# Kernel optimization log

Measured on AMD Instinct MI355X. Metric: run time of the kernel, lower is better.

Reference implementation:

```python
import jax, jax.numpy as jnp
import numpy as np

D = 256; NH = 8; NLEV = 4; NPTS = 4; DH = D // NH
DFFN = 1024; B = 8; LQ = 900
SHAPES = np.array([[100, 100], [50, 50], [25, 25], [13, 13]], dtype=np.int64)
STARTS = np.concatenate([[0], np.cumsum(SHAPES[:, 0] * SHAPES[:, 1])[:-1]]).astype(np.int64)
LEN = int((SHAPES[:, 0] * SHAPES[:, 1]).sum())


def _ln(x, w, b, eps=1e-5):
    m = x.mean(-1, keepdims=True)
    v = ((x - m) ** 2).mean(-1, keepdims=True)
    return (x - m) / jnp.sqrt(v + eps) * w + b


def _msdeform(q, ref, src, val_w, val_b, off_w, off_b, aw_w, aw_b, op_w, op_b):
    # Multi-scale deformable attention (Deformable DETR core), grid_sample
    # bilinear / zeros padding / align_corners=False semantics.
    Bq, Lq = q.shape[0], q.shape[1]
    value = (src @ val_w + val_b).reshape(Bq, -1, NH, DH)
    off = (q @ off_w + off_b).reshape(Bq, Lq, NH, NLEV, NPTS, 2)
    aw = jax.nn.softmax((q @ aw_w + aw_b).reshape(Bq, Lq, NH, NLEV * NPTS), -1)
    aw = aw.reshape(Bq, Lq, NH, NLEV, NPTS)
    norm = jnp.asarray(SHAPES[:, ::-1].copy(), dtype=q.dtype)  # (W_l, H_l)
    loc = ref[:, :, None, :, None, :] + off / norm[None, None, None, :, None, :]
    out = jnp.zeros((Bq, Lq, NH, DH), q.dtype)
    for l in range(NLEV):
        Hl, Wl = int(SHAPES[l, 0]), int(SHAPES[l, 1]); s = int(STARTS[l])
        v = value[:, s:s + Hl * Wl]                  # [B, Hl*Wl, NH, DH]
        lx = loc[:, :, :, l, :, 0] * Wl - 0.5        # align_corners=False pixel coords
        ly = loc[:, :, :, l, :, 1] * Hl - 0.5        # [B, Lq, NH, NPTS]
        x0 = jnp.floor(lx); y0 = jnp.floor(ly)
        fx = lx - x0; fy = ly - y0
        x0 = x0.astype(jnp.int32); y0 = y0.astype(jnp.int32)
        samp = jnp.zeros((Bq, Lq, NH, NPTS, DH), q.dtype)
        for dx, dy in ((0, 0), (1, 0), (0, 1), (1, 1)):
            xi = x0 + dx; yi = y0 + dy
            w = (fx if dx else 1.0 - fx) * (fy if dy else 1.0 - fy)
            valid = (xi >= 0) & (xi < Wl) & (yi >= 0) & (yi < Hl)
            idx = jnp.clip(yi, 0, Hl - 1) * Wl + jnp.clip(xi, 0, Wl - 1)
            idx_f = idx.transpose(0, 1, 3, 2).reshape(Bq, Lq * NPTS, NH)
            g = jnp.take_along_axis(v, idx_f[..., None], axis=1)
            g = g.reshape(Bq, Lq, NPTS, NH, DH).transpose(0, 1, 3, 2, 4)
            samp = samp + jnp.where(valid, w, 0.0)[..., None] * g
        out = out + jnp.sum(samp * aw[:, :, :, l, :, None], axis=3)
    return out.reshape(Bq, Lq, D) @ op_w + op_b


def _forward(tgt, query_pos, reference_points, src, qkv_w, qkv_b, out_w, out_b,
             ln2_w, ln2_b, val_w, val_b, off_w, off_b, aw_w, aw_b, op_w, op_b,
             ln1_w, ln1_b, w1, b1, w2, b2, ln3_w, ln3_b):
    Bq, Lq, _ = tgt.shape
    # --- self attention: q=k=tgt+pos, value=tgt (eval mode, no dropout) ---
    q = tgt + query_pos
    wq, wk, wv = qkv_w[:, :D], qkv_w[:, D:2 * D], qkv_w[:, 2 * D:]
    bq, bk, bv = qkv_b[:D], qkv_b[D:2 * D], qkv_b[2 * D:]
    qh = (q @ wq + bq).reshape(Bq, Lq, NH, DH)
    kh = (q @ wk + bk).reshape(Bq, Lq, NH, DH)
    vh = (tgt @ wv + bv).reshape(Bq, Lq, NH, DH)
    scores = jnp.einsum('bqhd,bkhd->bhqk', qh, kh) / jnp.sqrt(jnp.asarray(DH, tgt.dtype))
    attn = jax.nn.softmax(scores, -1)
    sa = jnp.einsum('bhqk,bkhd->bqhd', attn, vh).reshape(Bq, Lq, D) @ out_w + out_b
    tgt = _ln(tgt + sa, ln2_w, ln2_b)
    # --- multi-scale deformable cross attention ---
    ca = _msdeform(tgt + query_pos, reference_points, src,
                   val_w, val_b, off_w, off_b, aw_w, aw_b, op_w, op_b)
    tgt = _ln(tgt + ca, ln1_w, ln1_b)
    # --- FFN ---
    ff = jax.nn.relu(tgt @ w1 + b1) @ w2 + b2
    return _ln(tgt + ff, ln3_w, ln3_b)


def setup_inputs():
    key = jax.random.key(0)
    ks = jax.random.split(key, 16)
    s = 0.02
    return {
        'tgt': jax.random.normal(ks[0], (B, LQ, D), jnp.float32),
        'query_pos': jax.random.normal(ks[1], (B, LQ, D), jnp.float32),
        'reference_points': jax.random.uniform(ks[2], (B, LQ, NLEV, 2), jnp.float32),
        'src': jax.random.normal(ks[3], (B, LEN, D), jnp.float32),
        'spatial_shapes': jnp.asarray(SHAPES),
        'level_start_index': jnp.asarray(STARTS),
        'qkv_w': jax.random.normal(ks[4], (D, 3 * D), jnp.float32) * s,
        'qkv_b': jnp.zeros((3 * D,), jnp.float32),
        'out_w': jax.random.normal(ks[5], (D, D), jnp.float32) * s,
        'out_b': jnp.zeros((D,), jnp.float32),
        'ln2_w': jnp.ones((D,), jnp.float32), 'ln2_b': jnp.zeros((D,), jnp.float32),
        'val_w': jax.random.normal(ks[6], (D, D), jnp.float32) * s,
        'val_b': jnp.zeros((D,), jnp.float32),
        'off_w': jax.random.normal(ks[7], (D, NH * NLEV * NPTS * 2), jnp.float32) * s,
        'off_b': jax.random.normal(ks[8], (NH * NLEV * NPTS * 2,), jnp.float32) * 0.5,
        'aw_w': jax.random.normal(ks[9], (D, NH * NLEV * NPTS), jnp.float32) * s,
        'aw_b': jnp.zeros((NH * NLEV * NPTS,), jnp.float32),
        'op_w': jax.random.normal(ks[10], (D, D), jnp.float32) * s,
        'op_b': jnp.zeros((D,), jnp.float32),
        'ln1_w': jnp.ones((D,), jnp.float32), 'ln1_b': jnp.zeros((D,), jnp.float32),
        'w1': jax.random.normal(ks[11], (D, DFFN), jnp.float32) * s,
        'b1': jnp.zeros((DFFN,), jnp.float32),
        'w2': jax.random.normal(ks[12], (DFFN, D), jnp.float32) * s,
        'b2': jnp.zeros((D,), jnp.float32),
        'ln3_w': jnp.ones((D,), jnp.float32), 'ln3_b': jnp.zeros((D,), jnp.float32),
    }


def reference(tgt, query_pos, reference_points, src, spatial_shapes, level_start_index,
              qkv_w, qkv_b, out_w, out_b, ln2_w, ln2_b, val_w, val_b, off_w, off_b,
              aw_w, aw_b, op_w, op_b, ln1_w, ln1_b, w1, b1, w2, b2, ln3_w, ln3_b):
    return _forward(tgt, query_pos, reference_points, src, qkv_w, qkv_b, out_w, out_b,
                    ln2_w, ln2_b, val_w, val_b, off_w, off_b, aw_w, aw_b, op_w, op_b,
                    ln1_w, ln1_b, w1, b1, w2, b2, ln3_w, ln3_b)
```

## Files before the change

kernel.cpp:

```cpp
#include <hip/hip_runtime.h>
#include <math.h>

#define Dm    256
#define NHm   8
#define DHm   32
#define NLEVm 4
#define NPTSm 4
#define DFFNm 1024
#define Bm    8
#define LQm   900
#define LENm  13294
#define MQ    (Bm * LQm)
#define MV    (Bm * LENm)
#define MQP   7296
#define MVP   106368
#define LQP   960

typedef __attribute__((ext_vector_type(8))) short short8;
typedef __attribute__((ext_vector_type(4))) float f32x4;

__device__ __forceinline__ unsigned short f2bf(float f) {
    unsigned int b = __float_as_uint(f);
    unsigned int r = (b + 0x7FFFu + ((b >> 16) & 1u)) >> 16;
    return (unsigned short)r;
}
__device__ __forceinline__ float bf2f(unsigned short u) {
    return __uint_as_float(((unsigned int)u) << 16);
}

__global__ __launch_bounds__(256) void prep0(const float* __restrict__ tgt,
                                             const float* __restrict__ qpos,
                                             unsigned short* __restrict__ tgtb,
                                             unsigned short* __restrict__ qb,
                                             int n4, int n4pad) {
    int i = blockIdx.x * blockDim.x + threadIdx.x;
    int stride = gridDim.x * blockDim.x;
    for (; i < n4pad; i += stride) {
        ushort4 ut, uq;
        if (i < n4) {
            float4 x = reinterpret_cast<const float4*>(tgt)[i];
            float4 y = reinterpret_cast<const float4*>(qpos)[i];
            ut.x = f2bf(x.x); ut.y = f2bf(x.y); ut.z = f2bf(x.z); ut.w = f2bf(x.w);
            uq.x = f2bf(x.x + y.x); uq.y = f2bf(x.y + y.y);
            uq.z = f2bf(x.z + y.z); uq.w = f2bf(x.w + y.w);
        } else {
            ut.x = ut.y = ut.z = ut.w = 0;
            uq.x = uq.y = uq.z = uq.w = 0;
        }
        reinterpret_cast<ushort4*>(tgtb)[i] = ut;
        reinterpret_cast<ushort4*>(qb)[i] = uq;
    }
}

__device__ __forceinline__ void wt_tile(const float* __restrict__ W,
                                        unsigned short* __restrict__ BT,
                                        int N, int K, int n0, int k0, int t,
                                        float (*tile)[65]) {
    #pragma unroll
    for (int r0 = 0; r0 < 64; r0 += 16) {
        int r = r0 + (t >> 4);
        int c = (t & 15) * 4;
        float4 v = *reinterpret_cast<const float4*>(W + (size_t)(k0 + r) * N + n0 + c);
        tile[r][c + 0] = v.x; tile[r][c + 1] = v.y; tile[r][c + 2] = v.z; tile[r][c + 3] = v.w;
    }
    __syncthreads();
    #pragma unroll
    for (int s = t; s < 512; s += 256) {
        int r = s >> 3, c8 = (s & 7) * 8;
        short8 u;
        #pragma unroll
        for (int j = 0; j < 8; ++j) u[j] = (short)f2bf(tile[c8 + j][r]);
        *reinterpret_cast<short8*>(BT + (size_t)(n0 + r) * K + k0 + c8) = u;
    }
}

__global__ __launch_bounds__(256) void wt_all(
        const float* __restrict__ qkv_w, const float* __restrict__ out_w,
        const float* __restrict__ val_w, const float* __restrict__ off_w,
        const float* __restrict__ aw_w,  const float* __restrict__ op_w,
        const float* __restrict__ w1,    const float* __restrict__ w2,
        unsigned short* __restrict__ BT_qkv, unsigned short* __restrict__ BT_out,
        unsigned short* __restrict__ BT_val, unsigned short* __restrict__ BT_off,
        unsigned short* __restrict__ BT_aw,  unsigned short* __restrict__ BT_op,
        unsigned short* __restrict__ BT_w1,  unsigned short* __restrict__ BT_w2) {
    __shared__ float tile[64][65];
    int bid = blockIdx.x;
    int t = threadIdx.x;
    const float* W; unsigned short* BT; int N, K, idx;
    if      (bid < 48)  { W = qkv_w; BT = BT_qkv; N = 768;  K = 256;  idx = bid; }
    else if (bid < 64)  { W = out_w; BT = BT_out; N = 256;  K = 256;  idx = bid - 48; }
    else if (bid < 80)  { W = val_w; BT = BT_val; N = 256;  K = 256;  idx = bid - 64; }
    else if (bid < 96)  { W = off_w; BT = BT_off; N = 256;  K = 256;  idx = bid - 80; }
    else if (bid < 104) { W = aw_w;  BT = BT_aw;  N = 128;  K = 256;  idx = bid - 96; }
    else if (bid < 120) { W = op_w;  BT = BT_op;  N = 256;  K = 256;  idx = bid - 104; }
    else if (bid < 184) { W = w1;    BT = BT_w1;  N = 1024; K = 256;  idx = bid - 120; }
    else                { W = w2;    BT = BT_w2;  N = 256;  K = 1024; idx = bid - 184; }
    int nt = N / 64;
    int n0 = (idx % nt) * 64, k0 = (idx / nt) * 64;
    wt_tile(W, BT, N, K, n0, k0, t, tile);
}

__device__ __forceinline__ void mfma_step(const unsigned short* Ac, const unsigned short* Bc,
                                          int wr, int wc, int l, f32x4 acc[4][4]) {
    short8 af[4], bfr[4];
    #pragma unroll
    for (int m = 0; m < 4; ++m)
        af[m] = *(const short8*)(Ac + (wr + m * 16 + (l & 15)) * 32 + (l >> 4) * 8);
    #pragma unroll
    for (int n = 0; n < 4; ++n)
        bfr[n] = *(const short8*)(Bc + (wc + n * 16 + (l & 15)) * 32 + (l >> 4) * 8);
    #pragma unroll
    for (int m = 0; m < 4; ++m)
        #pragma unroll
        for (int n = 0; n < 4; ++n)
            acc[m][n] = __builtin_amdgcn_mfma_f32_16x16x32_bf16(af[m], bfr[n], acc[m][n], 0, 0, 0);
}

template <int RELU, int OBF>
__global__ __launch_bounds__(256) void bgemm(int M, int N, int K,
        const unsigned short* __restrict__ A,
        const unsigned short* __restrict__ BT,
        const float* __restrict__ bias, const float* __restrict__ bias2,
        float* __restrict__ Cf, float* __restrict__ Cf2,
        unsigned short* __restrict__ Cb, int ldc) {
    __shared__ __align__(16) unsigned short As[2][128 * 32];
    __shared__ __align__(16) unsigned short Bs[2][128 * 32];
    int t = threadIdx.x;
    int l = t & 63;
    int w = t >> 6;
    int row0 = blockIdx.x * 128, col0 = blockIdx.y * 128;
    int wr = (w >> 1) * 64, wc = (w & 1) * 64;
    f32x4 acc[4][4];
    #pragma unroll
    for (int m = 0; m < 4; ++m)
        #pragma unroll
        for (int n = 0; n < 4; ++n) acc[m][n] = (f32x4){0.f, 0.f, 0.f, 0.f};

    int s0 = t, s1 = t + 256;
    const unsigned short* Ag = A + (size_t)row0 * K;
    const unsigned short* Bg = BT + (size_t)col0 * K;
    const unsigned short* a0p = Ag + (size_t)(s0 >> 2) * K + (s0 & 3) * 8;
    const unsigned short* a1p = Ag + (size_t)(s1 >> 2) * K + (s1 & 3) * 8;
    const unsigned short* b0p = Bg + (size_t)(s0 >> 2) * K + (s0 & 3) * 8;
    const unsigned short* b1p = Bg + (size_t)(s1 >> 2) * K + (s1 & 3) * 8;

    short8 ra0 = *(const short8*)(a0p);
    short8 ra1 = *(const short8*)(a1p);
    short8 rb0 = *(const short8*)(b0p);
    short8 rb1 = *(const short8*)(b1p);

    int cur = 0;
    for (int k0 = 0; k0 < K; k0 += 32) {
        unsigned short* Ac = As[cur];
        unsigned short* Bc = Bs[cur];
        *(short8*)(Ac + s0 * 8) = ra0;
        *(short8*)(Ac + s1 * 8) = ra1;
        *(short8*)(Bc + s0 * 8) = rb0;
        *(short8*)(Bc + s1 * 8) = rb1;
        if (k0 + 32 < K) {
            ra0 = *(const short8*)(a0p + k0 + 32);
            ra1 = *(const short8*)(a1p + k0 + 32);
            rb0 = *(const short8*)(b0p + k0 + 32);
            rb1 = *(const short8*)(b1p + k0 + 32);
        }
        __syncthreads();
        mfma_step(Ac, Bc, wr, wc, l, acc);
        cur ^= 1;
    }

    int cr = (l >> 4) * 4;
    int cc = l & 15;
    #pragma unroll
    for (int m = 0; m < 4; ++m) {
        #pragma unroll
        for (int n = 0; n < 4; ++n) {
            int col = col0 + wc + n * 16 + cc;
            if (OBF == 3) {
                float bv = (col < 256) ? bias[col] : bias2[col - 256];
                #pragma unroll
                for (int j = 0; j < 4; ++j) {
                    int r = row0 + wr + m * 16 + cr + j;
                    if (r < M) {
                        float v = acc[m][n][j] + bv;
                        if (col < 256) Cf[(size_t)r * 256 + col] = v;
                        else           Cf2[(size_t)r * 128 + (col - 256)] = v;
                    }
                }
            } else {
                float bv = bias[col];
                #pragma unroll
                for (int j = 0; j < 4; ++j) {
                    int r = row0 + wr + m * 16 + cr + j;
                    if (r < M) {
                        float v = acc[m][n][j] + bv;
                        if (RELU) v = fmaxf(v, 0.f);
                        if (OBF) Cb[(size_t)r * ldc + col] = f2bf(v);
                        else     Cf[(size_t)r * ldc + col] = v;
                    }
                }
            }
        }
    }
}

__global__ __launch_bounds__(256) void fused_gemms(
        const float* __restrict__ src, const unsigned short* __restrict__ BT_val,
        const float* __restrict__ val_b, unsigned short* __restrict__ value_bf,
        const unsigned short* __restrict__ Qbf, const unsigned short* __restrict__ BT_qkv,
        const float* __restrict__ qkv_b, unsigned short* __restrict__ qk_bf,
        const unsigned short* __restrict__ tgt_bf, unsigned short* __restrict__ Vt) {
    __shared__ __align__(16) unsigned short As[2][128 * 32];
    __shared__ __align__(16) unsigned short Bs[2][128 * 32];
    int bid = blockIdx.x;
    int t = threadIdx.x;

    if (bid >= 2004) {
        int i = (bid - 2004) * 256 + t;
        int row = i / 60, c = 900 + (i % 60);
        Vt[(size_t)row * LQP + c] = 0;
        return;
    }

    int l = t & 63, w = t >> 6;
    int wr = (w >> 1) * 64, wc = (w & 1) * 64;
    int s0 = t, s1 = t + 256;
    f32x4 acc[4][4];
    #pragma unroll
    for (int m = 0; m < 4; ++m)
        #pragma unroll
        for (int n = 0; n < 4; ++n) acc[m][n] = (f32x4){0.f, 0.f, 0.f, 0.f};
    int cr = (l >> 4) * 4;
    int cc = l & 15;

    if (bid < 1662) {
        int row0 = (bid % 831) * 128, col0 = (bid / 831) * 128;
        int r0c = min(row0 + (s0 >> 2), MV - 1);
        int r1c = min(row0 + (s1 >> 2), MV - 1);
        const float* a0p = src + (size_t)r0c * 256 + (s0 & 3) * 8;
        const float* a1p = src + (size_t)r1c * 256 + (s1 & 3) * 8;
        const unsigned short* Bg = BT_val + (size_t)col0 * 256;
        const unsigned short* b0p = Bg + (size_t)(s0 >> 2) * 256 + (s0 & 3) * 8;
        const unsigned short* b1p = Bg + (size_t)(s1 >> 2) * 256 + (s1 & 3) * 8;

        float4 fa0 = *(const float4*)(a0p);
        float4 fa1 = *(const float4*)(a0p + 4);
        float4 fb0 = *(const float4*)(a1p);
        float4 fb1 = *(const float4*)(a1p + 4);
        short8 rb0 = *(const short8*)(b0p);
        short8 rb1 = *(const short8*)(b1p);

        int cur = 0;
        for (int k0 = 0; k0 < 256; k0 += 32) {
            unsigned short* Ac = As[cur];
            unsigned short* Bc = Bs[cur];
            short8 ra0, ra1;
            ra0[0] = (short)f2bf(fa0.x); ra0[1] = (short)f2bf(fa0.y);
            ra0[2] = (short)f2bf(fa0.z); ra0[3] = (short)f2bf(fa0.w);
            ra0[4] = (short)f2bf(fa1.x); ra0[5] = (short)f2bf(fa1.y);
            ra0[6] = (short)f2bf(fa1.z); ra0[7] = (short)f2bf(fa1.w);
            ra1[0] = (short)f2bf(fb0.x); ra1[1] = (short)f2bf(fb0.y);
            ra1[2] = (short)f2bf(fb0.z); ra1[3] = (short)f2bf(fb0.w);
            ra1[4] = (short)f2bf(fb1.x); ra1[5] = (short)f2bf(fb1.y);
            ra1[6] = (short)f2bf(fb1.z); ra1[7] = (short)f2bf(fb1.w);
            *(short8*)(Ac + s0 * 8) = ra0;
            *(short8*)(Ac + s1 * 8) = ra1;
            *(short8*)(Bc + s0 * 8) = rb0;
            *(short8*)(Bc + s1 * 8) = rb1;
            if (k0 + 32 < 256) {
                fa0 = *(const float4*)(a0p + k0 + 32);
                fa1 = *(const float4*)(a0p + k0 + 36);
                fb0 = *(const float4*)(a1p + k0 + 32);
                fb1 = *(const float4*)(a1p + k0 + 36);
                rb0 = *(const short8*)(b0p + k0 + 32);
                rb1 = *(const short8*)(b1p + k0 + 32);
            }
            __syncthreads();
            mfma_step(Ac, Bc, wr, wc, l, acc);
            cur ^= 1;
        }
        #pragma unroll
        for (int m = 0; m < 4; ++m) {
            #pragma unroll
            for (int n = 0; n < 4; ++n) {
                int col = col0 + wc + n * 16 + cc;
                float bv = val_b[col];
                #pragma unroll
                for (int j = 0; j < 4; ++j) {
                    int r = row0 + wr + m * 16 + cr + j;
                    if (r < MV)
                        value_bf[(size_t)r * 256 + col] = f2bf(acc[m][n][j] + bv);
                }
            }
        }
    } else {
        bool is_qk = (bid < 1890);
        int idx = is_qk ? (bid - 1662) : (bid - 1890);
        int row0 = (idx % 57) * 128;
        int col0 = (idx / 57) * 128;
        const unsigned short* A  = is_qk ? Qbf : tgt_bf;
        const unsigned short* BT = is_qk ? BT_qkv : (BT_qkv + 512 * 256);
        const float* bias        = is_qk ? qkv_b : (qkv_b + 512);

        const unsigned short* Ag = A + (size_t)row0 * 256;
        const unsigned short* Bg = BT + (size_t)col0 * 256;
        const unsigned short* a0p = Ag + (size_t)(s0 >> 2) * 256 + (s0 & 3) * 8;
        const unsigned short* a1p = Ag + (size_t)(s1 >> 2) * 256 + (s1 & 3) * 8;
        const unsigned short* b0p = Bg + (size_t)(s0 >> 2) * 256 + (s0 & 3) * 8;
        const unsigned short* b1p = Bg + (size_t)(s1 >> 2) * 256 + (s1 & 3) * 8;

        short8 ra0 = *(const short8*)(a0p);
        short8 ra1 = *(const short8*)(a1p);
        short8 rb0 = *(const short8*)(b0p);
        short8 rb1 = *(const short8*)(b1p);

        int cur = 0;
        for (int k0 = 0; k0 < 256; k0 += 32) {
            unsigned short* Ac = As[cur];
            unsigned short* Bc = Bs[cur];
            *(short8*)(Ac + s0 * 8) = ra0;
            *(short8*)(Ac + s1 * 8) = ra1;
            *(short8*)(Bc + s0 * 8) = rb0;
            *(short8*)(Bc + s1 * 8) = rb1;
            if (k0 + 32 < 256) {
                ra0 = *(const short8*)(a0p + k0 + 32);
                ra1 = *(const short8*)(a1p + k0 + 32);
                rb0 = *(const short8*)(b0p + k0 + 32);
                rb1 = *(const short8*)(b1p + k0 + 32);
            }
            __syncthreads();
            mfma_step(Ac, Bc, wr, wc, l, acc);
            cur ^= 1;
        }

        if (is_qk) {
            #pragma unroll
            for (int m = 0; m < 4; ++m) {
                #pragma unroll
                for (int n = 0; n < 4; ++n) {
                    int col = col0 + wc + n * 16 + cc;
                    float bv = bias[col];
                    #pragma unroll
                    for (int j = 0; j < 4; ++j) {
                        int r = row0 + wr + m * 16 + cr + j;
                        if (r < MQ)
                            qk_bf[(size_t)r * 512 + col] = f2bf(acc[m][n][j] + bv);
                    }
                }
            }
        } else {
            #pragma unroll
            for (int m = 0; m < 4; ++m) {
                #pragma unroll
                for (int n = 0; n < 4; ++n) {
                    int col = col0 + wc + n * 16 + cc;
                    float bv = bias[col];
                    int r0 = row0 + wr + m * 16 + cr;
                    if (r0 < MQ) {
                        int bb = r0 / 900;
                        int q = r0 - bb * 900;
                        ushort4 u;
                        u.x = f2bf(acc[m][n][0] + bv);
                        u.y = f2bf(acc[m][n][1] + bv);
                        u.z = f2bf(acc[m][n][2] + bv);
                        u.w = f2bf(acc[m][n][3] + bv);
                        *reinterpret_cast<ushort4*>(Vt + ((size_t)(bb * 256 + col)) * LQP + q) = u;
                    }
                }
            }
        }
    }
}

__global__ __launch_bounds__(256) void flash_mfma(const unsigned short* __restrict__ qk,
                                                  const unsigned short* __restrict__ vt,
                                                  unsigned short* __restrict__ out) {
    __shared__ unsigned short P_lds[4][16][72];
    int t = threadIdx.x;
    int l = t & 63, w = t >> 6;
    int lr = l & 15, lg = l >> 4;
    int qt = blockIdx.x, h = blockIdx.y, b = blockIdx.z;
    const float scale = 0.17677669529663687f;

    short8 qf = *(const short8*)(qk + (size_t)(b * LQm + qt * 64 + w * 16 + lr) * 512 + h * 32 + lg * 8);

    f32x4 accO[2];
    accO[0] = (f32x4){0.f, 0.f, 0.f, 0.f};
    accO[1] = (f32x4){0.f, 0.f, 0.f, 0.f};
    float mrow[4] = {-1e30f, -1e30f, -1e30f, -1e30f};
    float lrow[4] = {0.f, 0.f, 0.f, 0.f};
    const f32x4 zero = (f32x4){0.f, 0.f, 0.f, 0.f};
    const unsigned short* vtb = vt + ((size_t)(b * 256 + h * 32)) * LQP;

    for (int kt = 0; kt < 15; ++kt) {
        int k0 = kt * 64;
        f32x4 sfr[4];
        #pragma unroll
        for (int ks = 0; ks < 4; ++ks) {
            short8 kf = *(const short8*)(qk + (size_t)(b * LQm + k0 + ks * 16 + lr) * 512 + 256 + h * 32 + lg * 8);
            sfr[ks] = __builtin_amdgcn_mfma_f32_16x16x32_bf16(qf, kf, zero, 0, 0, 0);
        }
        float sv[4][4];
        #pragma unroll
        for (int ks = 0; ks < 4; ++ks) {
            bool valid = (k0 + ks * 16 + lr) < LQm;
            #pragma unroll
            for (int j = 0; j < 4; ++j)
                sv[ks][j] = valid ? sfr[ks][j] * scale : -1e30f;
        }
        float tm[4], newm[4], rr[4], ps[4];
        #pragma unroll
        for (int j = 0; j < 4; ++j)
            tm[j] = fmaxf(fmaxf(sv[0][j], sv[1][j]), fmaxf(sv[2][j], sv[3][j]));
        #pragma unroll
        for (int msk = 1; msk <= 8; msk <<= 1) {
            #pragma unroll
            for (int j = 0; j < 4; ++j) tm[j] = fmaxf(tm[j], __shfl_xor(tm[j], msk));
        }
        #pragma unroll
        for (int j = 0; j < 4; ++j) {
            newm[j] = fmaxf(mrow[j], tm[j]);
            rr[j] = __expf(mrow[j] - newm[j]);
            mrow[j] = newm[j];
            ps[j] = 0.f;
        }
        float pv[4][4];
        #pragma unroll
        for (int ks = 0; ks < 4; ++ks)
            #pragma unroll
            for (int j = 0; j < 4; ++j) {
                pv[ks][j] = __expf(sv[ks][j] - newm[j]);
                ps[j] += pv[ks][j];
            }
        #pragma unroll
        for (int msk = 1; msk <= 8; msk <<= 1) {
            #pragma unroll
            for (int j = 0; j < 4; ++j) ps[j] += __shfl_xor(ps[j], msk);
        }
        #pragma unroll
        for (int j = 0; j < 4; ++j) lrow[j] = lrow[j] * rr[j] + ps[j];
        #pragma unroll
        for (int n = 0; n < 2; ++n)
            #pragma unroll
            for (int j = 0; j < 4; ++j) accO[n][j] *= rr[j];
        #pragma unroll
        for (int ks = 0; ks < 4; ++ks)
            #pragma unroll
            for (int j = 0; j < 4; ++j)
                P_lds[w][lg * 4 + j][ks * 16 + lr] = f2bf(pv[ks][j]);
        #pragma unroll
        for (int kh2 = 0; kh2 < 2; ++kh2) {
            short8 pf = *(const short8*)(&P_lds[w][lr][kh2 * 32 + lg * 8]);
            #pragma unroll
            for (int n = 0; n < 2; ++n) {
                short8 vf = *(const short8*)(vtb + (size_t)(n * 16 + lr) * LQP + k0 + kh2 * 32 + lg * 8);
                accO[n] = __builtin_amdgcn_mfma_f32_16x16x32_bf16(pf, vf, accO[n], 0, 0, 0);
            }
        }
    }
    float inv[4];
    #pragma unroll
    for (int j = 0; j < 4; ++j) inv[j] = 1.0f / lrow[j];
    #pragma unroll
    for (int n = 0; n < 2; ++n)
        #pragma unroll
        for (int j = 0; j < 4; ++j) {
            int q = qt * 64 + w * 16 + lg * 4 + j;
            if (q < LQm)
                out[(size_t)(b * LQm + q) * 256 + h * 32 + n * 16 + lr] = f2bf(accO[n][j] * inv[j]);
        }
}

template <int DUAL, int QP>
__global__ __launch_bounds__(256) void add_ln_kernel(const float* __restrict__ x,
                                                     const float* __restrict__ r,
                                                     const float* __restrict__ w,
                                                     const float* __restrict__ b,
                                                     const float* __restrict__ qpos,
                                                     float* __restrict__ out,
                                                     unsigned short* __restrict__ outb,
                                                     unsigned short* __restrict__ outq) {
    int row = blockIdx.x * 4 + (threadIdx.x >> 6);
    int lane = threadIdx.x & 63;
    size_t i4 = (size_t)row * 64 + lane;
    float4 xv = reinterpret_cast<const float4*>(x)[i4];
    float4 rv = reinterpret_cast<const float4*>(r)[i4];
    float4 v = make_float4(xv.x + rv.x, xv.y + rv.y, xv.z + rv.z, xv.w + rv.w);
    float s = v.x + v.y + v.z + v.w;
    #pragma unroll
    for (int msk = 1; msk <= 32; msk <<= 1) s += __shfl_xor(s, msk);
    float mean = s * (1.0f / Dm);
    float4 dv = make_float4(v.x - mean, v.y - mean, v.z - mean, v.w - mean);
    float sq = dv.x * dv.x + dv.y * dv.y + dv.z * dv.z + dv.w * dv.w;
    #pragma unroll
    for (int msk = 1; msk <= 32; msk <<= 1) sq += __shfl_xor(sq, msk);
    float is = rsqrtf(sq * (1.0f / Dm) + 1e-5f);
    float4 wv = reinterpret_cast<const float4*>(w)[lane];
    float4 bv = reinterpret_cast<const float4*>(b)[lane];
    float4 res = make_float4(dv.x * is * wv.x + bv.x, dv.y * is * wv.y + bv.y,
                             dv.z * is * wv.z + bv.z, dv.w * is * wv.w + bv.w);
    reinterpret_cast<float4*>(out)[i4] = res;
    if (DUAL) {
        ushort4 u;
        u.x = f2bf(res.x); u.y = f2bf(res.y); u.z = f2bf(res.z); u.w = f2bf(res.w);
        reinterpret_cast<ushort4*>(outb)[i4] = u;
    }
    if (QP) {
        float4 qv = reinterpret_cast<const float4*>(qpos)[i4];
        ushort4 u;
        u.x = f2bf(res.x + qv.x); u.y = f2bf(res.y + qv.y);
        u.z = f2bf(res.z + qv.z); u.w = f2bf(res.w + qv.w);
        reinterpret_cast<ushort4*>(outq)[i4] = u;
    }
}

__global__ __launch_bounds__(256) void msdeform_kernel(const unsigned short* __restrict__ value,
                                                       const float* __restrict__ ref,
                                                       const float* __restrict__ off,
                                                       const float* __restrict__ awl,
                                                       unsigned short* __restrict__ out) {
    const int HL[4] = {100, 50, 25, 13};
    const int ST[4] = {0, 10000, 12500, 13125};
    __shared__ float lsx[4][128], lsy[4][128], wtab[4][128];
    __shared__ float2 ctab[4][512];
    int wv = threadIdx.x >> 6, lane = threadIdx.x & 63;
    int m = blockIdx.x * 4 + wv;
    int b = m / LQm;

    #pragma unroll
    for (int e = lane; e < 128; e += 64) {
        int lev = (e >> 2) & 3;
        float rx = ref[((size_t)m * NLEVm + lev) * 2 + 0];
        float ry = ref[((size_t)m * NLEVm + lev) * 2 + 1];
        float ox = off[(size_t)m * 256 + e * 2 + 0];
        float oy = off[(size_t)m * 256 + e * 2 + 1];
        float Wf = (float)HL[lev];
        lsx[wv][e] = (rx + ox / Wf) * Wf - 0.5f;
        lsy[wv][e] = (ry + oy / Wf) * Wf - 0.5f;
        wtab[wv][e] = awl[(size_t)m * 128 + e];
    }
    __syncthreads();
    if (lane < NHm) {
        int h = lane;
        float mx = -1e30f;
        #pragma unroll
        for (int i = 0; i < 16; i++) mx = fmaxf(mx, wtab[wv][h * 16 + i]);
        float s = 0.f;
        #pragma unroll
        for (int i = 0; i < 16; i++) {
            float e = __expf(wtab[wv][h * 16 + i] - mx);
            wtab[wv][h * 16 + i] = e; s += e;
        }
        float inv = 1.0f / s;
        #pragma unroll
        for (int i = 0; i < 16; i++) wtab[wv][h * 16 + i] *= inv;
    }
    __syncthreads();
    #pragma unroll
    for (int j = 0; j < 8; ++j) {
        int e2 = lane * 8 + j;
        int c = e2 & 3, e = e2 >> 2;
        int lev = (e >> 2) & 3;
        int Wl = HL[lev];
        float lx = lsx[wv][e], ly = lsy[wv][e];
        float x0f = floorf(lx), y0f = floorf(ly);
        float fx = lx - x0f, fy = ly - y0f;
        int dx = c & 1, dy = c >> 1;
        int xi = (int)x0f + dx, yi = (int)y0f + dy;
        bool valid = (xi >= 0) && (xi < Wl) && (yi >= 0) && (yi < Wl);
        float wc = valid ? ((dx ? fx : 1.0f - fx) * (dy ? fy : 1.0f - fy)) * wtab[wv][e] : 0.f;
        int xc = min(max(xi, 0), Wl - 1), yc = min(max(yi, 0), Wl - 1);
        int row = b * LENm + ST[lev] + yc * Wl + xc;
        ctab[wv][e2] = make_float2(__int_as_float(row), wc);
    }
    __syncthreads();
    int h = lane >> 3, dg = lane & 7;
    const unsigned short* basep = value + h * 32 + dg * 4;
    float a0 = 0.f, a1 = 0.f, a2 = 0.f, a3 = 0.f;
    #pragma unroll
    for (int i = 0; i < 16; ++i) {
        #pragma unroll
        for (int c = 0; c < 4; ++c) {
            float2 cc = ctab[wv][(h * 16 + i) * 4 + c];
            int row = __float_as_int(cc.x);
            float wc = cc.y;
            ushort4 v = *reinterpret_cast<const ushort4*>(basep + (size_t)row * 256);
            a0 += wc * bf2f(v.x); a1 += wc * bf2f(v.y);
            a2 += wc * bf2f(v.z); a3 += wc * bf2f(v.w);
        }
    }
    ushort4 o;
    o.x = f2bf(a0); o.y = f2bf(a1); o.z = f2bf(a2); o.w = f2bf(a3);
    *reinterpret_cast<ushort4*>(out + (size_t)m * 256 + h * 32 + dg * 4) = o;
}

extern "C" void kernel_launch(void* const* d_in, const int* in_sizes, int n_in,
                              void* d_out, int out_size, void* d_ws, size_t ws_size,
                              hipStream_t stream) {
    const float* tgt   = (const float*)d_in[0];
    const float* qpos  = (const float*)d_in[1];
    const float* refp  = (const float*)d_in[2];
    const float* src   = (const float*)d_in[3];
    const float* qkv_w = (const float*)d_in[6];
    const float* qkv_b = (const float*)d_in[7];
    const float* out_w = (const float*)d_in[8];
    const float* out_b = (const float*)d_in[9];
    const float* ln2_w = (const float*)d_in[10];
    const float* ln2_b = (const float*)d_in[11];
    const float* val_w = (const float*)d_in[12];
    const float* val_b = (const float*)d_in[13];
    const float* off_w = (const float*)d_in[14];
    const float* off_b = (const float*)d_in[15];
    const float* aw_w  = (const float*)d_in[16];
    const float* aw_b  = (const float*)d_in[17];
    const float* op_w  = (const float*)d_in[18];
    const float* op_b  = (const float*)d_in[19];
    const float* ln1_w = (const float*)d_in[20];
    const float* ln1_b = (const float*)d_in[21];
    const float* w1    = (const float*)d_in[22];
    const float* b1    = (const float*)d_in[23];
    const float* w2    = (const float*)d_in[24];
    const float* b2    = (const float*)d_in[25];
    const float* ln3_w = (const float*)d_in[26];
    const float* ln3_b = (const float*)d_in[27];

    char* base = (char*)d_ws;
    unsigned short* value_bf  = (unsigned short*)(base);
    unsigned short* hidden_bf = (unsigned short*)(base + 54460416);
    unsigned short* t2_bf     = (unsigned short*)(base + 54460416 + 14942208);
    unsigned short* qk_bf = (unsigned short*)(base + 108920832);
    float* offb = (float*)(base + 108920832);
    float* awb  = (float*)(base + 108920832 + 7372800);
    unsigned short* Vt = (unsigned short*)(base + 123666432);
    float* S1   = (float*)(base + 123666432);
    float* t1   = (float*)(base + 131039232);
    float* t2   = (float*)(base + 138412032);
    unsigned short* Qbf     = (unsigned short*)(base + 145784832);
    unsigned short* tgt_bf  = (unsigned short*)(base + 149520384);
    unsigned short* attn_bf = (unsigned short*)(base + 153255936);
    unsigned short* ca_bf   = (unsigned short*)(base + 156991488);
    unsigned short* BT_qkv  = (unsigned short*)(base + 160727040);
    unsigned short* BT_out  = BT_qkv + 768 * 256;
    unsigned short* BT_val  = BT_out + 256 * 256;
    unsigned short* BT_off  = BT_val + 256 * 256;
    unsigned short* BT_aw   = BT_off + 256 * 256;
    unsigned short* BT_op   = BT_aw + 128 * 256;
    unsigned short* BT_w1   = BT_op + 256 * 256;
    unsigned short* BT_w2   = BT_w1 + 1024 * 256;
    float* outp = (float*)d_out;

    dim3 blk(256);
    wt_all<<<dim3(248), blk, 0, stream>>>(qkv_w, out_w, val_w, off_w, aw_w, op_w, w1, w2,
                                          BT_qkv, BT_out, BT_val, BT_off, BT_aw, BT_op, BT_w1, BT_w2);
    prep0<<<dim3(1824), blk, 0, stream>>>(tgt, qpos, tgt_bf, Qbf, MQ * Dm / 4, MQP * Dm / 4);

    fused_gemms<<<dim3(2484), blk, 0, stream>>>(src, BT_val, val_b, value_bf,
                                                Qbf, BT_qkv, qkv_b, qk_bf, tgt_bf, Vt);

    flash_mfma<<<dim3(15, NHm, Bm), blk, 0, stream>>>(qk_bf, Vt, attn_bf);
    bgemm<0, 0><<<dim3(57, 2), blk, 0, stream>>>(MQ, 256, 256, attn_bf, BT_out, out_b, nullptr, S1, nullptr, nullptr, 256);
    add_ln_kernel<0, 1><<<dim3(1800), blk, 0, stream>>>(tgt, S1, ln2_w, ln2_b, qpos, t1, nullptr, Qbf);
    bgemm<0, 3><<<dim3(57, 3), blk, 0, stream>>>(MQ, 384, 256, Qbf, BT_off, off_b, aw_b, offb, awb, nullptr, 0);
    msdeform_kernel<<<dim3(1800), blk, 0, stream>>>(value_bf, refp, offb, awb, ca_bf);
    bgemm<0, 0><<<dim3(57, 2), blk, 0, stream>>>(MQ, 256, 256, ca_bf, BT_op, op_b, nullptr, S1, nullptr, nullptr, 256);
    add_ln_kernel<1, 0><<<dim3(1800), blk, 0, stream>>>(t1, S1, ln1_w, ln1_b, nullptr, t2, t2_bf, nullptr);
    bgemm<1, 1><<<dim3(57, 8), blk, 0, stream>>>(MQ, DFFNm, 256, t2_bf, BT_w1, b1, nullptr, nullptr, nullptr, hidden_bf, DFFNm);
    bgemm<0, 0><<<dim3(57, 2), blk, 0, stream>>>(MQ, 256, 1024, hidden_bf, BT_w2, b2, nullptr, S1, nullptr, nullptr, 256);
    add_ln_kernel<0, 0><<<dim3(1800), blk, 0, stream>>>(t2, S1, ln3_w, ln3_b, nullptr, outp, nullptr, nullptr);
}
```

Before: 251.4 us.

## Load GEMM tiles directly into LDS and convert value operand from fp32 in LDS

Replaces the register-staged, double-buffered global-to-LDS tile loads in the fused GEMM kernel with direct global_load_lds 16-byte transfers. The value projection now stores raw fp32 source tiles in LDS using an XOR swizzle and converts them to bf16 when building MFMA fragments, rather than converting before the LDS store. The aim is to cut VGPR staging and store instructions. The cost is losing the software prefetch overlap: each k-step now issues its loads and then waits at a barrier before computing, and the fp32 A tile doubles its LDS footprint.

```diff
diff --git a/kernel.cpp b/kernel.cpp
--- a/kernel.cpp
+++ b/kernel.cpp
@@ -26,6 +26,13 @@
 }
 __device__ __forceinline__ float bf2f(unsigned short u) {
     return __uint_as_float(((unsigned int)u) << 16);
+}
+
+__device__ __forceinline__ void gload16(const void* g, void* l) {
+    __builtin_amdgcn_global_load_lds(
+        (const __attribute__((address_space(1))) unsigned int*)g,
+        (__attribute__((address_space(3))) unsigned int*)l,
+        16, 0, 0);
 }
 
 __global__ __launch_bounds__(256) void prep0(const float* __restrict__ tgt,
@@ -209,8 +216,8 @@
         const unsigned short* __restrict__ Qbf, const unsigned short* __restrict__ BT_qkv,
         const float* __restrict__ qkv_b, unsigned short* __restrict__ qk_bf,
         const unsigned short* __restrict__ tgt_bf, unsigned short* __restrict__ Vt) {
-    __shared__ __align__(16) unsigned short As[2][128 * 32];
-    __shared__ __align__(16) unsigned short Bs[2][128 * 32];
+    __shared__ __align__(16) unsigned char AsRaw[16384];
+    __shared__ __align__(16) unsigned short Bs[128 * 32];
     int bid = blockIdx.x;
     int t = threadIdx.x;
 
@@ -222,61 +229,63 @@
     }
 
     int l = t & 63, w = t >> 6;
+    int lr = l & 15, lg = l >> 4;
     int wr = (w >> 1) * 64, wc = (w & 1) * 64;
-    int s0 = t, s1 = t + 256;
     f32x4 acc[4][4];
     #pragma unroll
     for (int m = 0; m < 4; ++m)
         #pragma unroll
         for (int n = 0; n < 4; ++n) acc[m][n] = (f32x4){0.f, 0.f, 0.f, 0.f};
-    int cr = (l >> 4) * 4;
-    int cc = l & 15;
+    int cr = lg * 4;
+    int cc = lr;
 
     if (bid < 1662) {
         int row0 = (bid % 831) * 128, col0 = (bid / 831) * 128;
-        int r0c = min(row0 + (s0 >> 2), MV - 1);
-        int r1c = min(row0 + (s1 >> 2), MV - 1);
-        const float* a0p = src + (size_t)r0c * 256 + (s0 & 3) * 8;
-        const float* a1p = src + (size_t)r1c * 256 + (s1 & 3) * 8;
-        const unsigned short* Bg = BT_val + (size_t)col0 * 256;
-        const unsigned short* b0p = Bg + (size_t)(s0 >> 2) * 256 + (s0 & 3) * 8;
-        const unsigned short* b1p = Bg + (size_t)(s1 >> 2) * 256 + (s1 & 3) * 8;
-
-        float4 fa0 = *(const float4*)(a0p);
-        float4 fa1 = *(const float4*)(a0p + 4);
-        float4 fb0 = *(const float4*)(a1p);
-        float4 fb1 = *(const float4*)(a1p + 4);
-        short8 rb0 = *(const short8*)(b0p);
-        short8 rb1 = *(const short8*)(b1p);
-
-        int cur = 0;
+        const float* asrc[4];
+        #pragma unroll
+        for (int i = 0; i < 4; ++i) {
+            int s = i * 256 + t;
+            int rloc = s >> 3;
+            int u = (s & 7) ^ (rloc & 7);
+            int r = min(row0 + rloc, MV - 1);
+            asrc[i] = src + (size_t)r * 256 + u * 4;
+        }
+        const unsigned short* bsrc[2];
+        #pragma unroll
+        for (int i = 0; i < 2; ++i) {
+            int s = i * 256 + t;
+            bsrc[i] = BT_val + (size_t)(col0 + (s >> 2)) * 256 + (s & 3) * 8;
+        }
+        const float* Asf = (const float*)AsRaw;
         for (int k0 = 0; k0 < 256; k0 += 32) {
-            unsigned short* Ac = As[cur];
-            unsigned short* Bc = Bs[cur];
-            short8 ra0, ra1;
-            ra0[0] = (short)f2bf(fa0.x); ra0[1] = (short)f2bf(fa0.y);
-            ra0[2] = (short)f2bf(fa0.z); ra0[3] = (short)f2bf(fa0.w);
-            ra0[4] = (short)f2bf(fa1.x); ra0[5] = (short)f2bf(fa1.y);
-            ra0[6] = (short)f2bf(fa1.z); ra0[7] = (short)f2bf(fa1.w);
-            ra1[0] = (short)f2bf(fb0.x); ra1[1] = (short)f2bf(fb0.y);
-            ra1[2] = (short)f2bf(fb0.z); ra1[3] = (short)f2bf(fb0.w);
-            ra1[4] = (short)f2bf(fb1.x); ra1[5] = (short)f2bf(fb1.y);
-            ra1[6] = (short)f2bf(fb1.z); ra1[7] = (short)f2bf(fb1.w);
-            *(short8*)(Ac + s0 * 8) = ra0;
-            *(short8*)(Ac + s1 * 8) = ra1;
-            *(short8*)(Bc + s0 * 8) = rb0;
-            *(short8*)(Bc + s1 * 8) = rb1;
-            if (k0 + 32 < 256) {
-                fa0 = *(const float4*)(a0p + k0 + 32);
-                fa1 = *(const float4*)(a0p + k0 + 36);
-                fb0 = *(const float4*)(a1p + k0 + 32);
-                fb1 = *(const float4*)(a1p + k0 + 36);
-                rb0 = *(const short8*)(b0p + k0 + 32);
-                rb1 = *(const short8*)(b1p + k0 + 32);
-            }
             __syncthreads();
-            mfma_step(Ac, Bc, wr, wc, l, acc);
-            cur ^= 1;
+            #pragma unroll
+            for (int i = 0; i < 4; ++i)
+                gload16(asrc[i] + k0, AsRaw + (i * 256 + w * 64) * 16);
+            #pragma unroll
+            for (int i = 0; i < 2; ++i)
+                gload16(bsrc[i] + k0, (unsigned char*)Bs + (i * 256 + w * 64) * 16);
+            __syncthreads();
+            short8 af[4], bfr[4];
+            #pragma unroll
+            for (int m = 0; m < 4; ++m) {
+                int row = wr + m * 16 + lr;
+                int sw = row & 7;
+                f32x4 v0 = *(const f32x4*)(Asf + row * 32 + ((lg * 2 + 0) ^ sw) * 4);
+                f32x4 v1 = *(const f32x4*)(Asf + row * 32 + ((lg * 2 + 1) ^ sw) * 4);
+                af[m][0] = (short)f2bf(v0[0]); af[m][1] = (short)f2bf(v0[1]);
+                af[m][2] = (short)f2bf(v0[2]); af[m][3] = (short)f2bf(v0[3]);
+                af[m][4] = (short)f2bf(v1[0]); af[m][5] = (short)f2bf(v1[1]);
+                af[m][6] = (short)f2bf(v1[2]); af[m][7] = (short)f2bf(v1[3]);
+            }
+            #pragma unroll
+            for (int n = 0; n < 4; ++n)
+                bfr[n] = *(const short8*)(Bs + (wc + n * 16 + lr) * 32 + lg * 8);
+            #pragma unroll
+            for (int m = 0; m < 4; ++m)
+                #pragma unroll
+                for (int n = 0; n < 4; ++n)
+                    acc[m][n] = __builtin_amdgcn_mfma_f32_16x16x32_bf16(af[m], bfr[n], acc[m][n], 0, 0, 0);
         }
         #pragma unroll
         for (int m = 0; m < 4; ++m) {
@@ -301,35 +310,24 @@
         const unsigned short* BT = is_qk ? BT_qkv : (BT_qkv + 512 * 256);
         const float* bias        = is_qk ? qkv_b : (qkv_b + 512);
 
-        const unsigned short* Ag = A + (size_t)row0 * 256;
-        const unsigned short* Bg = BT + (size_t)col0 * 256;
-        const unsigned short* a0p = Ag + (size_t)(s0 >> 2) * 256 + (s0 & 3) * 8;
-        const unsigned short* a1p = Ag + (size_t)(s1 >> 2) * 256 + (s1 & 3) * 8;
-        const unsigned short* b0p = Bg + (size_t)(s0 >> 2) * 256 + (s0 & 3) * 8;
-        const unsigned short* b1p = Bg + (size_t)(s1 >> 2) * 256 + (s1 & 3) * 8;
-
-        short8 ra0 = *(const short8*)(a0p);
-        short8 ra1 = *(const short8*)(a1p);
-        short8 rb0 = *(const short8*)(b0p);
-        short8 rb1 = *(const short8*)(b1p);
-
-        int cur = 0;
+        const unsigned short* asrc[2];
+        const unsigned short* bsrc[2];
+        #pragma unroll
+        for (int i = 0; i < 2; ++i) {
+            int s = i * 256 + t;
+            asrc[i] = A  + (size_t)(row0 + (s >> 2)) * 256 + (s & 3) * 8;
+            bsrc[i] = BT + (size_t)(col0 + (s >> 2)) * 256 + (s & 3) * 8;
+        }
+        unsigned short* Asb = (unsigned short*)AsRaw;
         for (int k0 = 0; k0 < 256; k0 += 32) {
-            unsigned short* Ac = As[cur];
-            unsigned short* Bc = Bs[cur];
-            *(short8*)(Ac + s0 * 8) = ra0;
-            *(short8*)(Ac + s1 * 8) = ra1;
-            *(short8*)(Bc + s0 * 8) = rb0;
-            *(short8*)(Bc + s1 * 8) = rb1;
-            if (k0 + 32 < 256) {
-                ra0 = *(const short8*)(a0p + k0 + 32);
-                ra1 = *(const short8*)(a1p + k0 + 32);
-                rb0 = *(const short8*)(b0p + k0 + 32);
-                rb1 = *(const short8*)(b1p + k0 + 32);
-            }
             __syncthreads();
-            mfma_step(Ac, Bc, wr, wc, l, acc);
-            cur ^= 1;
+            #pragma unroll
+            for (int i = 0; i < 2; ++i) {
+                gload16(asrc[i] + k0, AsRaw + (i * 256 + w * 64) * 16);
+                gload16(bsrc[i] + k0, (unsigned char*)Bs + (i * 256 + w * 64) * 16);
+            }
+            __syncthreads();
+            mfma_step(Asb, Bs, wr, wc, l, acc);
         }
 
         if (is_qk) {
```

Result: no change. 250.7 us (-0.3%).
